# Kernel optimization log

Measured on AMD Instinct MI355X. Metric: run time of the kernel, lower is better.

The kernel has to match this reference:

```python
import jax, jax.numpy as jnp
import numpy as np

DIM = 192
HEADS = 6
HIDDEN = 384  # int(DIM * 2.0)


def _ln(x, w, b):
    # WithBias LayerNorm over channel dim (torch normalizes last dim of b,(hw),c)
    mu = jnp.mean(x, axis=1, keepdims=True)
    var = jnp.var(x, axis=1, keepdims=True)
    return (x - mu) / jnp.sqrt(var + 1e-5) * w[None, :, None, None] + b[None, :, None, None]


def _conv1x1(x, w):  # w: [O, I, 1, 1]
    return jnp.einsum('bihw,oi->bohw', x, w[:, :, 0, 0])


def _dwconv3(x, w):  # depthwise 3x3, w: [C, 1, 3, 3]
    return jax.lax.conv_general_dilated(
        x, w, window_strides=(1, 1), padding=((1, 1), (1, 1)),
        feature_group_count=x.shape[1],
        dimension_numbers=('NCHW', 'OIHW', 'NCHW'))


def _l2norm(x):  # F.normalize along last axis
    n = jnp.sqrt(jnp.sum(x * x, axis=-1, keepdims=True))
    return x / jnp.maximum(n, 1e-12)


def setup_inputs() -> dict:
    key = jax.random.key(0)
    ks = jax.random.split(key, 16)
    s = 0.02
    d = {}
    d['x'] = jax.random.normal(ks[0], (2, DIM, 128, 128), dtype=jnp.float32)
    d['k_v'] = jax.random.normal(ks[1], (2, 256), dtype=jnp.float32)
    d['ln1_w'] = jnp.ones((DIM,), jnp.float32)
    d['ln1_b'] = jnp.zeros((DIM,), jnp.float32)
    d['temp'] = jnp.ones((HEADS, 1, 1), jnp.float32)
    d['w_kR'] = jax.random.normal(ks[2], (DIM * 3 // 4, 192), jnp.float32) * s
    d['w_kI'] = jax.random.normal(ks[3], (DIM // 4, 64), jnp.float32) * s
    d['w_qR'] = jax.random.normal(ks[4], (DIM, DIM * 3 // 4, 1, 1), jnp.float32) * s
    d['w_qdw'] = jax.random.normal(ks[5], (DIM, 1, 3, 3), jnp.float32) * s
    d['w_kvI'] = jax.random.normal(ks[6], (DIM * 2, DIM // 4, 1, 1), jnp.float32) * s
    d['w_kvdw'] = jax.random.normal(ks[7], (DIM * 2, 1, 3, 3), jnp.float32) * s
    d['w_po'] = jax.random.normal(ks[8], (DIM, DIM, 1, 1), jnp.float32) * s
    d['ln2_w'] = jnp.ones((DIM,), jnp.float32)
    d['ln2_b'] = jnp.zeros((DIM,), jnp.float32)
    d['w_ffk'] = jax.random.normal(ks[9], (DIM, 256), jnp.float32) * s
    d['w_pin'] = jax.random.normal(ks[10], (HIDDEN * 2, DIM, 1, 1), jnp.float32) * s
    d['w_dw'] = jax.random.normal(ks[11], (HIDDEN * 2, 1, 3, 3), jnp.float32) * s
    d['w_pout'] = jax.random.normal(ks[12], (DIM, HIDDEN, 1, 1), jnp.float32) * s
    return d


def reference(x, k_v, ln1_w, ln1_b, temp, w_kR, w_kI, w_qR, w_qdw, w_kvI, w_kvdw,
              w_po, ln2_w, ln2_b, w_ffk, w_pin, w_dw, w_pout):
    b, c, h, w = x.shape
    c3 = c * 3 // 4
    # ---- Rttention on norm1(x) ----
    xn = _ln(x, ln1_w, ln1_b)
    kvr = (k_v[:, :192] @ w_kR.T)[:, :, None, None]   # [b, 3c/4, 1, 1]
    kvi = (k_v[:, 192:] @ w_kI.T)[:, :, None, None]   # [b, c/4, 1, 1]
    x_r = xn[:, :c3] * kvr + xn[:, :c3]
    x_i = xn[:, c3:] * kvi + xn[:, c3:]
    q = _dwconv3(_conv1x1(x_r, w_qR), w_qdw)          # [b, c, h, w]
    kv = _dwconv3(_conv1x1(x_i, w_kvI), w_kvdw)       # [b, 2c, h, w]
    k, v = jnp.split(kv, 2, axis=1)
    rh = lambda t: t.reshape(b, HEADS, c // HEADS, h * w)
    q = _l2norm(rh(q))
    k = _l2norm(rh(k))
    v = rh(v)
    # channel-wise attention: [b, head, c_h, c_h]
    attn = jax.nn.softmax(jnp.einsum('bhcd,bhed->bhce', q, k) * temp[None], axis=-1)
    out = jnp.einsum('bhce,bhed->bhcd', attn, v).reshape(b, c, h, w)
    x = x + _conv1x1(out, w_po)
    # ---- GDFN FeedForward on norm2(x) ----
    xn2 = _ln(x, ln2_w, ln2_b)
    kvf = (k_v @ w_ffk.T)[:, :, None, None]           # [b, c, 1, 1]
    y = xn2 * kvf + xn2
    y = _dwconv3(_conv1x1(y, w_pin), w_dw)            # [b, 2*hidden, h, w]
    y1, y2 = jnp.split(y, 2, axis=1)
    y = jax.nn.gelu(y1, approximate=False) * y2
    x = x + _conv1x1(y, w_pout)
    return (x, k_v)
```

## Files before the change

### kernel.cpp

```cpp
#include <hip/hip_runtime.h>
#include <math.h>

#define HW 16384
#define CDIM 192
#define C3 144
#define C4 48
#define NB 2
#define NPX 32768
#define HEADS 6

typedef unsigned short u16;
typedef unsigned int u32;
typedef __attribute__((ext_vector_type(8))) short bf16x8;
typedef __attribute__((ext_vector_type(4))) float f32x4;

__device__ __forceinline__ float bf2f(u16 u) {
    return __uint_as_float(((unsigned int)u) << 16);
}
__device__ __forceinline__ u16 f2bf(float f) {
    unsigned int x = __float_as_uint(f);
    unsigned int r = x + 0x7fffu + ((x >> 16) & 1u);
    return (u16)(r >> 16);
}

static inline float* wsf(void* ws, size_t off) { return (float*)((char*)ws + off); }
static inline u16* wsh(void* ws, size_t off) { return (u16*)((char*)ws + off); }

__global__ void k_setup(const float* __restrict__ kvv, const float* __restrict__ wkR,
                        const float* __restrict__ wkI, const float* __restrict__ wffk,
                        const float* __restrict__ wqR, const float* __restrict__ wkvI,
                        const float* __restrict__ wpo, const float* __restrict__ wpin,
                        const float* __restrict__ wpout,
                        const float* __restrict__ ln2w, const float* __restrict__ ln2b,
                        u16* __restrict__ wb, float* __restrict__ sm,
                        float* __restrict__ A2, float* __restrict__ B2,
                        float* __restrict__ tail) {
    int t = blockIdx.x * 256 + threadIdx.x;
    if (t < 313344) {
        float v;
        if (t < 30720) {
            int o = t / 160, i = t % 160;
            v = (i < 144) ? wqR[o * 144 + i] : 0.f;
        } else if (t < 55296) {
            int r = t - 30720; int o = r / 64, i = r % 64;
            v = (i < 48) ? wkvI[o * 48 + i] : 0.f;
        } else if (t < 92160) {
            v = wpo[t - 55296];
        } else if (t < 239616) {
            v = wpin[t - 92160];
        } else {
            v = wpout[t - 239616];
        }
        wb[t] = f2bf(v);
    } else if (t < 314112) {
        int r = t - 313344;
        if (r < 288) {
            int b = r / 144, o = r % 144;
            const float* v = kvv + b * 256;
            const float* w = wkR + o * 192;
            float s = 0.f;
            for (int j = 0; j < 192; j++) s += v[j] * w[j];
            sm[r] = s + 1.0f;
        } else if (r < 384) {
            int r2 = r - 288;
            int b = r2 / 48, o = r2 % 48;
            const float* v = kvv + b * 256 + 192;
            const float* w = wkI + o * 64;
            float s = 0.f;
            for (int j = 0; j < 64; j++) s += v[j] * w[j];
            sm[288 + r2] = s + 1.0f;
        } else {
            int r2 = r - 384;
            int b = r2 / 192, o = r2 % 192;
            const float* v = kvv + b * 256;
            const float* w = wffk + o * 256;
            float s = 0.f;
            for (int j = 0; j < 256; j++) s += v[j] * w[j];
            float sc = s + 1.0f;
            sm[384 + r2] = sc;
            A2[r2] = ln2w[o] * sc;
            B2[r2] = ln2b[o] * sc;
        }
    } else if (t < 314624) {
        int r = t - 314112;
        tail[r] = kvv[r];
    }
}

__global__ __launch_bounds__(256) void k_ln1(
    const float* __restrict__ xin,
    const float* __restrict__ lnw, const float* __restrict__ lnb,
    const float* __restrict__ sca, const float* __restrict__ scb,
    u16* __restrict__ outA, u16* __restrict__ outB) {
    __shared__ float red[2][16][16][4];
    __shared__ float mu_s[16][4], rstd_s[16][4];
    int t = threadIdx.x;
    int px4 = t & 15, cg = t >> 4;
    int base = blockIdx.x * 64;
    int b = base >> 14;
    int p = (base & 16383) + px4 * 4;
    float vals[12][4];
    float s[4] = {0.f, 0.f, 0.f, 0.f}, s2[4] = {0.f, 0.f, 0.f, 0.f};
#pragma unroll
    for (int j = 0; j < 12; j++) {
        int c = cg * 12 + j;
        size_t off = ((size_t)(b * CDIM + c)) * HW + p;
        float4 f = *(const float4*)(xin + off);
        float v[4] = {f.x, f.y, f.z, f.w};
#pragma unroll
        for (int q = 0; q < 4; q++) {
            vals[j][q] = v[q]; s[q] += v[q]; s2[q] += v[q] * v[q];
        }
    }
#pragma unroll
    for (int q = 0; q < 4; q++) { red[0][cg][px4][q] = s[q]; red[1][cg][px4][q] = s2[q]; }
    __syncthreads();
    if (t < 16) {
        float S[4] = {0.f, 0.f, 0.f, 0.f}, S2[4] = {0.f, 0.f, 0.f, 0.f};
        for (int g2 = 0; g2 < 16; g2++)
#pragma unroll
            for (int q = 0; q < 4; q++) { S[q] += red[0][g2][t][q]; S2[q] += red[1][g2][t][q]; }
#pragma unroll
        for (int q = 0; q < 4; q++) {
            float mu = S[q] * (1.0f / CDIM);
            float var = S2[q] * (1.0f / CDIM) - mu * mu;
            mu_s[t][q] = mu;
            rstd_s[t][q] = rsqrtf(var + 1e-5f);
        }
    }
    __syncthreads();
    float mu[4], rs[4];
#pragma unroll
    for (int q = 0; q < 4; q++) { mu[q] = mu_s[px4][q]; rs[q] = rstd_s[px4][q]; }
    float Ac[12], Bc[12];
#pragma unroll
    for (int j = 0; j < 12; j++) {
        int c = cg * 12 + j;
        float sc = (c < C3) ? sca[b * C3 + c] : scb[b * C4 + (c - C3)];
        Ac[j] = lnw[c] * sc;
        Bc[j] = lnb[c] * sc;
    }
    int isR = (cg < 12);
    size_t row0 = (size_t)b * HW + p;
    u16* basep = isR ? (outA + row0 * 160 + cg * 12)
                     : (outB + row0 * 64 + (cg * 12 - 144));
    int rowlen = isR ? 160 : 64;
#pragma unroll
    for (int q = 0; q < 4; q++) {
        u16 tmp[12];
#pragma unroll
        for (int j = 0; j < 12; j++)
            tmp[j] = f2bf((vals[j][q] - mu[q]) * rs[q] * Ac[j] + Bc[j]);
        u16* op = basep + q * rowlen;
        ushort4 o0 = {tmp[0], tmp[1], tmp[2], tmp[3]};
        ushort4 o1 = {tmp[4], tmp[5], tmp[6], tmp[7]};
        ushort4 o2 = {tmp[8], tmp[9], tmp[10], tmp[11]};
        *(ushort4*)(op) = o0;
        *(ushort4*)(op + 4) = o1;
        *(ushort4*)(op + 8) = o2;
    }
    if (cg == 0) {
        int4 z = {0, 0, 0, 0};
#pragma unroll
        for (int q = 0; q < 4; q++) {
            u16* pr = outA + (row0 + q) * 160 + 144;
            *(int4*)(pr) = z; *(int4*)(pr + 8) = z;
            u16* pi = outB + (row0 + q) * 64 + 48;
            *(int4*)(pi) = z; *(int4*)(pi + 8) = z;
        }
    }
}

template <int NCH, int MODE>
__global__ __launch_bounds__(256, 4) void k_gemm_t(
    const u16* __restrict__ X, const u16* __restrict__ Wb,
    const void* __restrict__ resid, void* __restrict__ outp, int CO) {
    constexpr int CIP = NCH * 32;
    const int tid = threadIdx.x;
    const int n0 = blockIdx.x * 128;
    const int m0 = blockIdx.y * 64;
    const int b = blockIdx.z;
    const int wave = tid >> 6, lane = tid & 63;
    const int quad = lane >> 4, l16 = lane & 15;
    const u16* arow = Wb + (size_t)(m0 + l16) * CIP + quad * 8;
    const u16* brow = X + ((size_t)b * HW + n0 + wave * 32 + l16) * CIP + quad * 8;
    f32x4 acc[4][2] = {};
    bf16x8 A[3][4], B[3][2];
    auto gload = [&](int slot, int cc) {
        const int k0 = cc * 32;
        B[slot][0] = *(const bf16x8*)(brow + k0);
        B[slot][1] = *(const bf16x8*)(brow + 16 * CIP + k0);
        A[slot][0] = *(const bf16x8*)(arow + k0);
        A[slot][1] = *(const bf16x8*)(arow + 16 * CIP + k0);
        A[slot][2] = *(const bf16x8*)(arow + 32 * CIP + k0);
        A[slot][3] = *(const bf16x8*)(arow + 48 * CIP + k0);
    };
    gload(0, 0);
    gload(1, 1);
#pragma unroll
    for (int ch = 0; ch < NCH; ch++) {
        if (ch + 2 < NCH) gload((ch + 2) % 3, ch + 2);
        const int s = ch % 3;
#pragma unroll
        for (int mi = 0; mi < 4; mi++) {
            acc[mi][0] = __builtin_amdgcn_mfma_f32_16x16x32_bf16(A[s][mi], B[s][0], acc[mi][0], 0, 0, 0);
            acc[mi][1] = __builtin_amdgcn_mfma_f32_16x16x32_bf16(A[s][mi], B[s][1], acc[mi][1], 0, 0, 0);
        }
    }
#pragma unroll
    for (int mi = 0; mi < 4; mi++) {
#pragma unroll
        for (int ni = 0; ni < 2; ni++) {
            int c0 = m0 + mi * 16 + quad * 4;
            int px = n0 + wave * 32 + ni * 16 + l16;
            if (MODE == 0) {
                u16* ob = (u16*)outp + ((size_t)b * CO + c0) * HW + px;
#pragma unroll
                for (int r = 0; r < 4; r++) ob[(size_t)r * HW] = f2bf(acc[mi][ni][r]);
            } else {
                const float* rp = (const float*)resid + ((size_t)b * 192 + c0) * HW + px;
                ushort4 o;
                o.x = f2bf(acc[mi][ni][0] + rp[0]);
                o.y = f2bf(acc[mi][ni][1] + rp[(size_t)HW]);
                o.z = f2bf(acc[mi][ni][2] + rp[(size_t)2 * HW]);
                o.w = f2bf(acc[mi][ni][3] + rp[(size_t)3 * HW]);
                *(ushort4*)((u16*)outp + ((size_t)b * HW + px) * 192 + c0) = o;
            }
        }
    }
}

__global__ __launch_bounds__(256) void k_gemm_s(
    const u16* __restrict__ X, const u16* __restrict__ Wb,
    const u16* __restrict__ residT, float* __restrict__ outp) {
    constexpr int NCH = 12;
    constexpr int CIP = NCH * 32;
    __shared__ __align__(16) u16 Ws[64 * 32];
    __shared__ __align__(16) u16 Xs[32 * 130];
    const int tid = threadIdx.x;
    const int n0 = blockIdx.x * 128;
    const int m0 = blockIdx.y * 64;
    const int b = blockIdx.z;
    const u16* Xb = X + (size_t)b * 384 * HW + n0;
    const int wave = tid >> 6, lane = tid & 63;
    const int quad = lane >> 4, l16 = lane & 15;
    const int smr = tid >> 2, sk4 = tid & 3;
    const int skr = tid >> 3, sc0 = (tid & 7) * 16;
    f32x4 acc[4][2] = {};
    for (int ch = 0; ch < NCH; ch++) {
        const int k0 = ch * 32;
        if (ch) __syncthreads();
        {
            const int4 wv = *(const int4*)(Wb + (size_t)(m0 + smr) * CIP + k0 + sk4 * 8);
            *(int4*)&Ws[(smr << 5) + (((sk4 ^ (smr & 3)) & 3) << 3)] = wv;
        }
        {
            const u16* xc = Xb + (size_t)(k0 + skr) * HW + sc0;
            int4 r0 = *(const int4*)xc;
            int4 r1 = *(const int4*)(xc + 8);
            u32* dst = (u32*)&Xs[skr * 130 + sc0];
#pragma unroll
            for (int i = 0; i < 4; i++) dst[i] = ((const u32*)&r0)[i];
#pragma unroll
            for (int i = 0; i < 4; i++) dst[4 + i] = ((const u32*)&r1)[i];
        }
        __syncthreads();
        bf16x8 af[4];
#pragma unroll
        for (int mi = 0; mi < 4; mi++) {
            int row = mi * 16 + l16;
            af[mi] = *(const bf16x8*)&Ws[(row << 5) + ((quad ^ (row & 3)) << 3)];
        }
#pragma unroll
        for (int ni = 0; ni < 2; ni++) {
            int n = wave * 32 + ni * 16 + l16;
            bf16x8 bfr;
#pragma unroll
            for (int j = 0; j < 8; j++) bfr[j] = (short)Xs[(quad * 8 + j) * 130 + n];
#pragma unroll
            for (int mi = 0; mi < 4; mi++)
                acc[mi][ni] = __builtin_amdgcn_mfma_f32_16x16x32_bf16(af[mi], bfr, acc[mi][ni], 0, 0, 0);
        }
    }
#pragma unroll
    for (int mi = 0; mi < 4; mi++) {
#pragma unroll
        for (int ni = 0; ni < 2; ni++) {
            int c0 = m0 + mi * 16 + quad * 4;
            int px = n0 + wave * 32 + ni * 16 + l16;
            ushort4 rv = *(const ushort4*)(residT + ((size_t)b * HW + px) * 192 + c0);
            float* ob = outp + ((size_t)b * 192 + c0) * HW + px;
            ob[0] = acc[mi][ni][0] + bf2f(rv.x);
            ob[(size_t)HW] = acc[mi][ni][1] + bf2f(rv.y);
            ob[(size_t)2 * HW] = acc[mi][ni][2] + bf2f(rv.z);
            ob[(size_t)3 * HW] = acc[mi][ni][3] + bf2f(rv.w);
        }
    }
}

__global__ __launch_bounds__(256) void k_dw2(const u16* __restrict__ X,
                                             const float* __restrict__ Wd,
                                             u16* __restrict__ out, int C, int sqCh,
                                             float* __restrict__ sqp) {
    __shared__ float In[34 * 132];
    __shared__ float red[4];
    int bc = blockIdx.x >> 2, rt = blockIdx.x & 3;
    int b = bc / C, ch = bc % C;
    const u16* xb = X + (size_t)bc * HW;
    int t = threadIdx.x;
    int c0 = (t & 7) * 16;
    for (int r = t >> 3; r < 34; r += 32) {
        int y = rt * 32 - 1 + r;
        float* dst = &In[r * 132 + 1 + c0];
        if ((unsigned)y < 128u) {
            const u16* src = xb + y * 128 + c0;
            int4 r0 = *(const int4*)src;
            int4 r1 = *(const int4*)(src + 8);
            const u16* p0 = (const u16*)&r0;
            const u16* p1 = (const u16*)&r1;
#pragma unroll
            for (int i = 0; i < 8; i++) dst[i] = bf2f(p0[i]);
#pragma unroll
            for (int i = 0; i < 8; i++) dst[8 + i] = bf2f(p1[i]);
        } else {
#pragma unroll
            for (int i = 0; i < 16; i++) dst[i] = 0.f;
        }
    }
    if (t < 34) { In[t * 132] = 0.f; In[t * 132 + 129] = 0.f; }
    __syncthreads();
    const float* w = Wd + ch * 9;
    float w00 = w[0], w01 = w[1], w02 = w[2], w10 = w[3], w11 = w[4],
          w12 = w[5], w20 = w[6], w21 = w[7], w22 = w[8];
    int x = t & 127, rg = t >> 7;
    int base = rg * 16;
    float A2 = 0.f, A1 = 0.f, B1 = 0.f, ssq = 0.f;
    u16* ob = out + (size_t)bc * HW + (rt * 32 + base) * 128 + x;
#pragma unroll
    for (int r = 0; r < 18; r++) {
        const float* row = &In[(base + r) * 132 + x];
        float v0 = row[0], v1 = row[1], v2 = row[2];
        float h0 = w00 * v0 + w01 * v1 + w02 * v2;
        float h1 = w10 * v0 + w11 * v1 + w12 * v2;
        float h2 = w20 * v0 + w21 * v1 + w22 * v2;
        if (r >= 2) {
            float val = A2 + B1 + h2;
            ob[(size_t)(r - 2) * 128] = f2bf(val);
            ssq += val * val;
        }
        A2 = A1; A1 = h0; B1 = h1;
    }
    if (ch < sqCh) {
        for (int o = 32; o > 0; o >>= 1) ssq += __shfl_down(ssq, o, 64);
        int wid = t >> 6, lane = t & 63;
        if (lane == 0) red[wid] = ssq;
        __syncthreads();
        if (t == 0) sqp[((b * 192 + ch) << 2) | rt] = red[0] + red[1] + red[2] + red[3];
    }
}

__global__ __launch_bounds__(256) void k_dw_gelu2(const u16* __restrict__ G0,
                                                  const float* __restrict__ Wd,
                                                  u16* __restrict__ out) {
    __shared__ float In[2 * 34 * 132];
    int bc = blockIdx.x >> 2, rt = blockIdx.x & 3;
    int b = bc / 384, j = bc % 384;
    int t = threadIdx.x;
    int c0 = (t & 7) * 16;
    for (int pl = 0; pl < 2; pl++) {
        const u16* xb = G0 + ((size_t)b * 768 + pl * 384 + j) * HW;
        float* pla = &In[pl * 34 * 132];
        for (int r = t >> 3; r < 34; r += 32) {
            int y = rt * 32 - 1 + r;
            float* dst = &pla[r * 132 + 1 + c0];
            if ((unsigned)y < 128u) {
                const u16* src = xb + y * 128 + c0;
                int4 r0 = *(const int4*)src;
                int4 r1 = *(const int4*)(src + 8);
                const u16* p0 = (const u16*)&r0;
                const u16* p1 = (const u16*)&r1;
#pragma unroll
                for (int i = 0; i < 8; i++) dst[i] = bf2f(p0[i]);
#pragma unroll
                for (int i = 0; i < 8; i++) dst[8 + i] = bf2f(p1[i]);
            } else {
#pragma unroll
                for (int i = 0; i < 16; i++) dst[i] = 0.f;
            }
        }
        if (t < 34) { pla[t * 132] = 0.f; pla[t * 132 + 129] = 0.f; }
    }
    __syncthreads();
    const float* w1 = Wd + j * 9;
    const float* w2 = Wd + (384 + j) * 9;
    float a00 = w1[0], a01 = w1[1], a02 = w1[2], a10 = w1[3], a11 = w1[4],
          a12 = w1[5], a20 = w1[6], a21 = w1[7], a22 = w1[8];
    float b00 = w2[0], b01 = w2[1], b02 = w2[2], b10 = w2[3], b11 = w2[4],
          b12 = w2[5], b20 = w2[6], b21 = w2[7], b22 = w2[8];
    int x = t & 127, rg = t >> 7;
    int base = rg * 16;
    float A2a = 0.f, A1a = 0.f, B1a = 0.f;
    float A2b = 0.f, A1b = 0.f, B1b = 0.f;
    u16* ob = out + ((size_t)b * 384 + j) * HW + (rt * 32 + base) * 128 + x;
#pragma unroll
    for (int r = 0; r < 18; r++) {
        const float* r1p = &In[(base + r) * 132 + x];
        const float* r2p = r1p + 34 * 132;
        float u0 = r1p[0], u1 = r1p[1], u2 = r1p[2];
        float v0 = r2p[0], v1 = r2p[1], v2 = r2p[2];
        float h0a = a00 * u0 + a01 * u1 + a02 * u2;
        float h1a = a10 * u0 + a11 * u1 + a12 * u2;
        float h2a = a20 * u0 + a21 * u1 + a22 * u2;
        float h0b = b00 * v0 + b01 * v1 + b02 * v2;
        float h1b = b10 * v0 + b11 * v1 + b12 * v2;
        float h2b = b20 * v0 + b21 * v1 + b22 * v2;
        if (r >= 2) {
            float s1 = A2a + B1a + h2a;
            float s2 = A2b + B1b + h2b;
            float g = 0.5f * s1 * (1.0f + erff(s1 * 0.70710678118654752f));
            ob[(size_t)(r - 2) * 128] = f2bf(g * s2);
        }
        A2a = A1a; A1a = h0a; B1a = h1a;
        A2b = A1b; A1b = h0b; B1b = h1b;
    }
}

__global__ __launch_bounds__(256) void k_qk(const u16* __restrict__ qb_,
                                            const u16* __restrict__ kb_,
                                            float* __restrict__ Spart) {
    int bh = blockIdx.x >> 6, ds = blockIdx.x & 63;
    int b = bh / HEADS, h = bh % HEADS;
    int tid = threadIdx.x;
    int wave = tid >> 6, lane = tid & 63;
    int quad = lane >> 4, l16 = lane & 15;
    int tm = wave >> 1, tn = wave & 1;
    const u16* qrow = qb_ + ((size_t)(b * 192 + h * 32 + tm * 16 + l16)) * HW + ds * 256 + quad * 8;
    const u16* krow = kb_ + ((size_t)(b * 384 + h * 32 + tn * 16 + l16)) * HW + ds * 256 + quad * 8;
    f32x4 acc = {};
    bf16x8 qa[3], ka[3];
    auto ld = [&](int s, int cc) {
        qa[s] = *(const bf16x8*)(qrow + cc * 32);
        ka[s] = *(const bf16x8*)(krow + cc * 32);
    };
    ld(0, 0); ld(1, 1);
#pragma unroll
    for (int ch = 0; ch < 8; ch++) {
        if (ch + 2 < 8) ld((ch + 2) % 3, ch + 2);
        acc = __builtin_amdgcn_mfma_f32_16x16x32_bf16(qa[ch % 3], ka[ch % 3], acc, 0, 0, 0);
    }
    float* Sb = Spart + ((size_t)ds * 12 + bh) * 1024;
#pragma unroll
    for (int r = 0; r < 4; r++)
        Sb[(tm * 16 + quad * 4 + r) * 32 + tn * 16 + l16] = acc[r];
}

__global__ void k_softmax(const float* __restrict__ Spart, const float* __restrict__ sqqp,
                          const float* __restrict__ sqkp, const float* __restrict__ temp,
                          u16* __restrict__ attnb) {
    int row = blockIdx.x;
    int bh = row >> 5, c2 = row & 31;
    int b = bh / HEADS, h = bh % HEADS;
    int e = threadIdx.x;
    float l = -1e30f;
    if (e < 32) {
        float s = 0.f;
        for (int d = 0; d < 64; d++) s += Spart[((size_t)d * 12 + bh) * 1024 + c2 * 32 + e];
        const float* qp = sqqp + (b * 192 + h * 32 + c2) * 4;
        const float* kp = sqkp + (b * 192 + h * 32 + e) * 4;
        float nq = qp[0] + qp[1] + qp[2] + qp[3];
        float nk = kp[0] + kp[1] + kp[2] + kp[3];
        float invq = 1.0f / fmaxf(sqrtf(nq), 1e-12f);
        float invk = 1.0f / fmaxf(sqrtf(nk), 1e-12f);
        l = s * invq * invk * temp[h];
    }
    float m = l;
    for (int o = 32; o > 0; o >>= 1) m = fmaxf(m, __shfl_xor(m, o, 64));
    float ev = (e < 32) ? expf(l - m) : 0.f;
    float ssum = ev;
    for (int o = 32; o > 0; o >>= 1) ssum += __shfl_xor(ssum, o, 64);
    if (e < 32) attnb[bh * 1024 + c2 * 32 + e] = f2bf(ev / ssum);
}

__global__ __launch_bounds__(256) void k_av(const u16* __restrict__ attnb,
                                            const u16* __restrict__ kvb,
                                            u16* __restrict__ out) {
    __shared__ __align__(16) u16 Vs[32 * 130];
    int bh = blockIdx.x >> 7;
    int pt = blockIdx.x & 127;
    int b = bh / HEADS, h = bh % HEADS;
    int p0 = pt * 128;
    int t = threadIdx.x;
    {
        int e = t >> 3, c0 = (t & 7) * 16;
        const u16* src = kvb + ((size_t)(b * 384 + 192 + h * 32 + e)) * HW + p0 + c0;
        int4 r0 = *(const int4*)src;
        int4 r1 = *(const int4*)(src + 8);
        u32* dst = (u32*)&Vs[e * 130 + c0];
#pragma unroll
        for (int i = 0; i < 4; i++) dst[i] = ((const u32*)&r0)[i];
#pragma unroll
        for (int i = 0; i < 4; i++) dst[4 + i] = ((const u32*)&r1)[i];
    }
    __syncthreads();
    int wave = t >> 6, lane = t & 63;
    int quad = lane >> 4, l16 = lane & 15;
    f32x4 acc[2][2] = {};
    bf16x8 af[2];
#pragma unroll
    for (int tm = 0; tm < 2; tm++)
        af[tm] = *(const bf16x8*)(attnb + bh * 1024 + (tm * 16 + l16) * 32 + quad * 8);
#pragma unroll
    for (int nt = 0; nt < 2; nt++) {
        int n = wave * 32 + nt * 16 + l16;
        bf16x8 bfr;
#pragma unroll
        for (int j = 0; j < 8; j++) bfr[j] = (short)Vs[(quad * 8 + j) * 130 + n];
#pragma unroll
        for (int tm = 0; tm < 2; tm++)
            acc[tm][nt] = __builtin_amdgcn_mfma_f32_16x16x32_bf16(af[tm], bfr, acc[tm][nt], 0, 0, 0);
    }
#pragma unroll
    for (int tm = 0; tm < 2; tm++)
#pragma unroll
        for (int nt = 0; nt < 2; nt++) {
            int c0 = h * 32 + tm * 16 + quad * 4;
            int px = p0 + wave * 32 + nt * 16 + l16;
            ushort4 o;
            o.x = f2bf(acc[tm][nt][0]);
            o.y = f2bf(acc[tm][nt][1]);
            o.z = f2bf(acc[tm][nt][2]);
            o.w = f2bf(acc[tm][nt][3]);
            *(ushort4*)(out + ((size_t)b * HW + px) * 192 + c0) = o;
        }
}

__global__ __launch_bounds__(256) void k_ln2t(
    const u16* __restrict__ xin, const float* __restrict__ A2,
    const float* __restrict__ B2, u16* __restrict__ outp) {
    int t = threadIdx.x;
    int pxg = blockIdx.x * 64 + (t >> 2);
    int l2 = t & 3;
    int b = pxg >> 14;
    const u16* src = xin + (size_t)pxg * 192 + l2 * 48;
    float v[48];
    float s = 0.f, s2 = 0.f;
#pragma unroll
    for (int i = 0; i < 6; i++) {
        int4 r0 = *(const int4*)(src + i * 8);
        const u16* pp = (const u16*)&r0;
#pragma unroll
        for (int k = 0; k < 8; k++) {
            float f = bf2f(pp[k]);
            v[i * 8 + k] = f; s += f; s2 += f * f;
        }
    }
    s += __shfl_xor(s, 1, 64);  s += __shfl_xor(s, 2, 64);
    s2 += __shfl_xor(s2, 1, 64); s2 += __shfl_xor(s2, 2, 64);
    float mu = s * (1.0f / CDIM);
    float rstd = rsqrtf(s2 * (1.0f / CDIM) - mu * mu + 1e-5f);
    const float* Ap = A2 + b * 192 + l2 * 48;
    const float* Bp = B2 + b * 192 + l2 * 48;
    u16* dst = outp + (size_t)pxg * 192 + l2 * 48;
#pragma unroll
    for (int i = 0; i < 12; i++) {
        float4 a = *(const float4*)(Ap + i * 4);
        float4 bb = *(const float4*)(Bp + i * 4);
        ushort4 o;
        o.x = f2bf((v[i * 4 + 0] - mu) * rstd * a.x + bb.x);
        o.y = f2bf((v[i * 4 + 1] - mu) * rstd * a.y + bb.y);
        o.z = f2bf((v[i * 4 + 2] - mu) * rstd * a.z + bb.z);
        o.w = f2bf((v[i * 4 + 3] - mu) * rstd * a.w + bb.w);
        *(ushort4*)(dst + i * 4) = o;
    }
}

extern "C" void kernel_launch(void* const* d_in, const int* in_sizes, int n_in,
                              void* d_out, int out_size, void* d_ws, size_t ws_size,
                              hipStream_t stream) {
    const float* x     = (const float*)d_in[0];
    const float* k_v   = (const float*)d_in[1];
    const float* ln1w  = (const float*)d_in[2];
    const float* ln1b  = (const float*)d_in[3];
    const float* temp  = (const float*)d_in[4];
    const float* w_kR  = (const float*)d_in[5];
    const float* w_kI  = (const float*)d_in[6];
    const float* w_qR  = (const float*)d_in[7];
    const float* w_qdw = (const float*)d_in[8];
    const float* w_kvI = (const float*)d_in[9];
    const float* w_kvdw= (const float*)d_in[10];
    const float* w_po  = (const float*)d_in[11];
    const float* ln2w  = (const float*)d_in[12];
    const float* ln2b  = (const float*)d_in[13];
    const float* w_ffk = (const float*)d_in[14];
    const float* w_pin = (const float*)d_in[15];
    const float* w_dw  = (const float*)d_in[16];
    const float* w_pout= (const float*)d_in[17];
    float* out = (float*)d_out;

    const size_t MiB = 1048576ULL;
    u16*   q0b     = wsh(d_ws, 0);
    u16*   attnoutb= wsh(d_ws, 0);
    u16*   y0b     = wsh(d_ws, 0);
    u16*   kv0b    = wsh(d_ws, 12 * MiB);
    u16*   ybufb   = wsh(d_ws, 12 * MiB);
    u16*   x1b     = wsh(d_ws, 36 * MiB);
    u16*   qbuf_b  = wsh(d_ws, 48 * MiB);
    u16*   kvbuf_b = wsh(d_ws, 60 * MiB);
    u16*   xrb     = wsh(d_ws, 84 * MiB);
    u16*   xib     = wsh(d_ws, 94 * MiB);
    u16*   g0b     = wsh(d_ws, 98 * MiB);
    u16*   wb      = wsh(d_ws, 146 * MiB);
    float* sm      = wsf(d_ws, 147 * MiB);
    float* Spart   = wsf(d_ws, 0);
    u16* wq   = wb;
    u16* wkv  = wb + 30720;
    u16* wpo  = wb + 55296;
    u16* wpin = wb + 92160;
    u16* wpout= wb + 239616;
    float* kvr  = sm;
    float* kvi  = sm + 288;
    float* sqqp = sm + 768;
    float* sqkp = sm + 2304;
    u16*   attnb= (u16*)(sm + 3840);
    float* A2c  = sm + 10240;
    float* B2c  = sm + 10624;

    k_setup<<<1229, 256, 0, stream>>>(k_v, w_kR, w_kI, w_ffk, w_qR, w_kvI, w_po,
                                      w_pin, w_pout, ln2w, ln2b, wb, sm, A2c, B2c,
                                      out + (size_t)NB * CDIM * HW);
    k_ln1<<<NPX / 64, 256, 0, stream>>>(x, ln1w, ln1b, kvr, kvi, xrb, xib);
    k_gemm_t<5, 0><<<dim3(128, 3, 2), 256, 0, stream>>>(xrb, wq, nullptr, q0b, 192);
    k_gemm_t<2, 0><<<dim3(128, 6, 2), 256, 0, stream>>>(xib, wkv, nullptr, kv0b, 384);
    k_dw2<<<NB * 192 * 4, 256, 0, stream>>>(q0b, w_qdw, qbuf_b, 192, 192, sqqp);
    k_dw2<<<NB * 384 * 4, 256, 0, stream>>>(kv0b, w_kvdw, kvbuf_b, 384, 192, sqkp);
    k_qk<<<12 * 64, 256, 0, stream>>>(qbuf_b, kvbuf_b, Spart);
    k_softmax<<<384, 64, 0, stream>>>(Spart, sqqp, sqkp, temp, attnb);
    k_av<<<12 * 128, 256, 0, stream>>>(attnb, kvbuf_b, attnoutb);
    k_gemm_t<6, 1><<<dim3(128, 3, 2), 256, 0, stream>>>(attnoutb, wpo, x, x1b, 192);
    k_ln2t<<<NPX / 64, 256, 0, stream>>>(x1b, A2c, B2c, y0b);
    k_gemm_t<6, 0><<<dim3(128, 12, 2), 256, 0, stream>>>(y0b, wpin, nullptr, g0b, 768);
    k_dw_gelu2<<<NB * 384 * 4, 256, 0, stream>>>(g0b, w_dw, ybufb);
    k_gemm_s<<<dim3(128, 3, 2), 256, 0, stream>>>(ybufb, wpout, x1b, out);
}
```

Before: 311.4 us.

## Keep activation tile in registers and loop over output-channel tiles in GEMM

The transposed GEMM kernel now loads the full activation (B) fragment for all K chunks into registers once, then loops over several 64-row weight tiles inside the block instead of launching one block per M tile. This cuts repeated global reads of the activation data across blocks. The trade-offs are fewer blocks (grids shrink by 3-6x), higher register pressure (launch bounds lowered to 2 blocks per SM), and the loss of the triple-buffered A/B prefetch pipeline.

```diff
diff --git a/kernel.cpp b/kernel.cpp
--- a/kernel.cpp
+++ b/kernel.cpp
@@ -171,60 +171,59 @@
     }
 }
 
-template <int NCH, int MODE>
-__global__ __launch_bounds__(256, 4) void k_gemm_t(
+template <int NCH, int MLOOP, int MODE>
+__global__ __launch_bounds__(256, 2) void k_gemm_t(
     const u16* __restrict__ X, const u16* __restrict__ Wb,
     const void* __restrict__ resid, void* __restrict__ outp, int CO) {
     constexpr int CIP = NCH * 32;
     const int tid = threadIdx.x;
     const int n0 = blockIdx.x * 128;
-    const int m0 = blockIdx.y * 64;
     const int b = blockIdx.z;
     const int wave = tid >> 6, lane = tid & 63;
     const int quad = lane >> 4, l16 = lane & 15;
-    const u16* arow = Wb + (size_t)(m0 + l16) * CIP + quad * 8;
     const u16* brow = X + ((size_t)b * HW + n0 + wave * 32 + l16) * CIP + quad * 8;
-    f32x4 acc[4][2] = {};
-    bf16x8 A[3][4], B[3][2];
-    auto gload = [&](int slot, int cc) {
-        const int k0 = cc * 32;
-        B[slot][0] = *(const bf16x8*)(brow + k0);
-        B[slot][1] = *(const bf16x8*)(brow + 16 * CIP + k0);
-        A[slot][0] = *(const bf16x8*)(arow + k0);
-        A[slot][1] = *(const bf16x8*)(arow + 16 * CIP + k0);
-        A[slot][2] = *(const bf16x8*)(arow + 32 * CIP + k0);
-        A[slot][3] = *(const bf16x8*)(arow + 48 * CIP + k0);
-    };
-    gload(0, 0);
-    gload(1, 1);
+    bf16x8 Bf[NCH][2];
 #pragma unroll
     for (int ch = 0; ch < NCH; ch++) {
-        if (ch + 2 < NCH) gload((ch + 2) % 3, ch + 2);
-        const int s = ch % 3;
+        Bf[ch][0] = *(const bf16x8*)(brow + ch * 32);
+        Bf[ch][1] = *(const bf16x8*)(brow + 16 * CIP + ch * 32);
+    }
+#pragma unroll
+    for (int ml = 0; ml < MLOOP; ml++) {
+        const int m0 = (blockIdx.y * MLOOP + ml) * 64;
+        const u16* arow = Wb + (size_t)(m0 + l16) * CIP + quad * 8;
+        f32x4 acc[4][2] = {};
+#pragma unroll
+        for (int ch = 0; ch < NCH; ch++) {
+            bf16x8 af[4];
+#pragma unroll
+            for (int mi = 0; mi < 4; mi++)
+                af[mi] = *(const bf16x8*)(arow + mi * 16 * CIP + ch * 32);
+#pragma unroll
+            for (int mi = 0; mi < 4; mi++) {
+                acc[mi][0] = __builtin_amdgcn_mfma_f32_16x16x32_bf16(af[mi], Bf[ch][0], acc[mi][0], 0, 0, 0);
+                acc[mi][1] = __builtin_amdgcn_mfma_f32_16x16x32_bf16(af[mi], Bf[ch][1], acc[mi][1], 0, 0, 0);
+            }
+        }
 #pragma unroll
         for (int mi = 0; mi < 4; mi++) {
-            acc[mi][0] = __builtin_amdgcn_mfma_f32_16x16x32_bf16(A[s][mi], B[s][0], acc[mi][0], 0, 0, 0);
-            acc[mi][1] = __builtin_amdgcn_mfma_f32_16x16x32_bf16(A[s][mi], B[s][1], acc[mi][1], 0, 0, 0);
-        }
-    }
-#pragma unroll
-    for (int mi = 0; mi < 4; mi++) {
-#pragma unroll
-        for (int ni = 0; ni < 2; ni++) {
-            int c0 = m0 + mi * 16 + quad * 4;
-            int px = n0 + wave * 32 + ni * 16 + l16;
-            if (MODE == 0) {
-                u16* ob = (u16*)outp + ((size_t)b * CO + c0) * HW + px;
-#pragma unroll
-                for (int r = 0; r < 4; r++) ob[(size_t)r * HW] = f2bf(acc[mi][ni][r]);
-            } else {
-                const float* rp = (const float*)resid + ((size_t)b * 192 + c0) * HW + px;
-                ushort4 o;
-                o.x = f2bf(acc[mi][ni][0] + rp[0]);
-                o.y = f2bf(acc[mi][ni][1] + rp[(size_t)HW]);
-                o.z = f2bf(acc[mi][ni][2] + rp[(size_t)2 * HW]);
-                o.w = f2bf(acc[mi][ni][3] + rp[(size_t)3 * HW]);
-                *(ushort4*)((u16*)outp + ((size_t)b * HW + px) * 192 + c0) = o;
+#pragma unroll
+            for (int ni = 0; ni < 2; ni++) {
+                int c0 = m0 + mi * 16 + quad * 4;
+                int px = n0 + wave * 32 + ni * 16 + l16;
+                if (MODE == 0) {
+                    u16* ob = (u16*)outp + ((size_t)b * CO + c0) * HW + px;
+#pragma unroll
+                    for (int r = 0; r < 4; r++) ob[(size_t)r * HW] = f2bf(acc[mi][ni][r]);
+                } else {
+                    const float* rp = (const float*)resid + ((size_t)b * 192 + c0) * HW + px;
+                    ushort4 o;
+                    o.x = f2bf(acc[mi][ni][0] + rp[0]);
+                    o.y = f2bf(acc[mi][ni][1] + rp[(size_t)HW]);
+                    o.z = f2bf(acc[mi][ni][2] + rp[(size_t)2 * HW]);
+                    o.w = f2bf(acc[mi][ni][3] + rp[(size_t)3 * HW]);
+                    *(ushort4*)((u16*)outp + ((size_t)b * HW + px) * 192 + c0) = o;
+                }
             }
         }
     }
@@ -629,16 +628,16 @@
                                       w_pin, w_pout, ln2w, ln2b, wb, sm, A2c, B2c,
                                       out + (size_t)NB * CDIM * HW);
     k_ln1<<<NPX / 64, 256, 0, stream>>>(x, ln1w, ln1b, kvr, kvi, xrb, xib);
-    k_gemm_t<5, 0><<<dim3(128, 3, 2), 256, 0, stream>>>(xrb, wq, nullptr, q0b, 192);
-    k_gemm_t<2, 0><<<dim3(128, 6, 2), 256, 0, stream>>>(xib, wkv, nullptr, kv0b, 384);
+    k_gemm_t<5, 3, 0><<<dim3(128, 1, 2), 256, 0, stream>>>(xrb, wq, nullptr, q0b, 192);
+    k_gemm_t<2, 3, 0><<<dim3(128, 2, 2), 256, 0, stream>>>(xib, wkv, nullptr, kv0b, 384);
     k_dw2<<<NB * 192 * 4, 256, 0, stream>>>(q0b, w_qdw, qbuf_b, 192, 192, sqqp);
     k_dw2<<<NB * 384 * 4, 256, 0, stream>>>(kv0b, w_kvdw, kvbuf_b, 384, 192, sqkp);
     k_qk<<<12 * 64, 256, 0, stream>>>(qbuf_b, kvbuf_b, Spart);
     k_softmax<<<384, 64, 0, stream>>>(Spart, sqqp, sqkp, temp, attnb);
     k_av<<<12 * 128, 256, 0, stream>>>(attnb, kvbuf_b, attnoutb);
-    k_gemm_t<6, 1><<<dim3(128, 3, 2), 256, 0, stream>>>(attnoutb, wpo, x, x1b, 192);
+    k_gemm_t<6, 3, 1><<<dim3(128, 1, 2), 256, 0, stream>>>(attnoutb, wpo, x, x1b, 192);
     k_ln2t<<<NPX / 64, 256, 0, stream>>>(x1b, A2c, B2c, y0b);
-    k_gemm_t<6, 0><<<dim3(128, 12, 2), 256, 0, stream>>>(y0b, wpin, nullptr, g0b, 768);
+    k_gemm_t<6, 6, 0><<<dim3(128, 2, 2), 256, 0, stream>>>(y0b, wpin, nullptr, g0b, 768);
     k_dw_gelu2<<<NB * 384 * 4, 256, 0, stream>>>(g0b, w_dw, ybufb);
     k_gemm_s<<<dim3(128, 3, 2), 256, 0, stream>>>(ybufb, wpout, x1b, out);
 }
```

New measurement: 297.7 us. 1.05x faster.

## Stage GEMM operand tiles through LDS with register prefetch in k_gemm_t

Applied to the files above, without the earlier changes.

Each K-chunk of the X and weight tiles is now loaded cooperatively into padded shared memory, and every wave reads its MFMA fragments from LDS. Before, each wave fetched its operands straight from global memory with a 3-deep register pipeline, so all four waves loaded the same weight fragments redundantly. The next chunk is prefetched into registers while the current one is computed. The change adds two barriers per chunk and LDS traffic, and drops the occupancy hint from launch_bounds.

```diff
diff --git a/kernel.cpp b/kernel.cpp
--- a/kernel.cpp
+++ b/kernel.cpp
@@ -172,39 +172,48 @@
 }
 
 template <int NCH, int MODE>
-__global__ __launch_bounds__(256, 4) void k_gemm_t(
+__global__ __launch_bounds__(256) void k_gemm_t(
     const u16* __restrict__ X, const u16* __restrict__ Wb,
     const void* __restrict__ resid, void* __restrict__ outp, int CO) {
     constexpr int CIP = NCH * 32;
+    __shared__ __align__(16) u16 Xs[128 * 40];
+    __shared__ __align__(16) u16 Wsh[64 * 40];
     const int tid = threadIdx.x;
     const int n0 = blockIdx.x * 128;
     const int m0 = blockIdx.y * 64;
     const int b = blockIdx.z;
     const int wave = tid >> 6, lane = tid & 63;
     const int quad = lane >> 4, l16 = lane & 15;
-    const u16* arow = Wb + (size_t)(m0 + l16) * CIP + quad * 8;
-    const u16* brow = X + ((size_t)b * HW + n0 + wave * 32 + l16) * CIP + quad * 8;
+    const int spx = tid >> 1, sh = tid & 1;
+    const int swr = tid >> 2, swc = tid & 3;
+    const u16* xsrc = X + ((size_t)b * HW + n0 + spx) * CIP + sh * 16;
+    const u16* wsrc = Wb + (size_t)(m0 + swr) * CIP + swc * 8;
+    int4 xr0 = *(const int4*)(xsrc);
+    int4 xr1 = *(const int4*)(xsrc + 8);
+    int4 wr0 = *(const int4*)(wsrc);
     f32x4 acc[4][2] = {};
-    bf16x8 A[3][4], B[3][2];
-    auto gload = [&](int slot, int cc) {
-        const int k0 = cc * 32;
-        B[slot][0] = *(const bf16x8*)(brow + k0);
-        B[slot][1] = *(const bf16x8*)(brow + 16 * CIP + k0);
-        A[slot][0] = *(const bf16x8*)(arow + k0);
-        A[slot][1] = *(const bf16x8*)(arow + 16 * CIP + k0);
-        A[slot][2] = *(const bf16x8*)(arow + 32 * CIP + k0);
-        A[slot][3] = *(const bf16x8*)(arow + 48 * CIP + k0);
-    };
-    gload(0, 0);
-    gload(1, 1);
 #pragma unroll
     for (int ch = 0; ch < NCH; ch++) {
-        if (ch + 2 < NCH) gload((ch + 2) % 3, ch + 2);
-        const int s = ch % 3;
+        if (ch) __syncthreads();
+        *(int4*)&Xs[spx * 40 + sh * 16] = xr0;
+        *(int4*)&Xs[spx * 40 + sh * 16 + 8] = xr1;
+        *(int4*)&Wsh[swr * 40 + swc * 8] = wr0;
+        if (ch + 1 < NCH) {
+            xr0 = *(const int4*)(xsrc + (ch + 1) * 32);
+            xr1 = *(const int4*)(xsrc + (ch + 1) * 32 + 8);
+            wr0 = *(const int4*)(wsrc + (ch + 1) * 32);
+        }
+        __syncthreads();
+        bf16x8 af[4];
+#pragma unroll
+        for (int mi = 0; mi < 4; mi++)
+            af[mi] = *(const bf16x8*)&Wsh[(mi * 16 + l16) * 40 + quad * 8];
+        bf16x8 bf0 = *(const bf16x8*)&Xs[(wave * 32 + l16) * 40 + quad * 8];
+        bf16x8 bf1 = *(const bf16x8*)&Xs[(wave * 32 + 16 + l16) * 40 + quad * 8];
 #pragma unroll
         for (int mi = 0; mi < 4; mi++) {
-            acc[mi][0] = __builtin_amdgcn_mfma_f32_16x16x32_bf16(A[s][mi], B[s][0], acc[mi][0], 0, 0, 0);
-            acc[mi][1] = __builtin_amdgcn_mfma_f32_16x16x32_bf16(A[s][mi], B[s][1], acc[mi][1], 0, 0, 0);
+            acc[mi][0] = __builtin_amdgcn_mfma_f32_16x16x32_bf16(af[mi], bf0, acc[mi][0], 0, 0, 0);
+            acc[mi][1] = __builtin_amdgcn_mfma_f32_16x16x32_bf16(af[mi], bf1, acc[mi][1], 0, 0, 0);
         }
     }
 #pragma unroll
@@ -216,7 +225,7 @@
             if (MODE == 0) {
                 u16* ob = (u16*)outp + ((size_t)b * CO + c0) * HW + px;
 #pragma unroll
-                for (int r = 0; r < 4; r++) ob[(size_t)r * HW] = f2bf(acc[mi][ni][r]);
+                for (int rr = 0; rr < 4; rr++) ob[(size_t)rr * HW] = f2bf(acc[mi][ni][rr]);
             } else {
                 const float* rp = (const float*)resid + ((size_t)b * 192 + c0) * HW + px;
                 ushort4 o;
```

Result: faster. 262.4 us (-15.7%).
